# Optimization experiments

Hardware: AMD Instinct MI355X
Metric: run time of the kernel (lower is better)

## Reference

```python
import jax, jax.numpy as jnp
import numpy as np
from jax import lax

OUT_SCALE = 0.001


def setup_inputs() -> dict:
    key = jax.random.key(0)
    kz, kx = jax.random.split(key)
    z = jax.random.normal(kz, (64, 256, 7, 7), dtype=jnp.float32)
    x = jax.random.normal(kx, (64, 256, 31, 31), dtype=jnp.float32)
    return {"z": z, "x": x}


def reference(z, x):
    # depthwise cross-correlation: each (batch, channel) slice of z is slid
    # over the matching slice of x. Implemented as a grouped conv with
    # feature_group_count = B*C, exactly mirroring torch F.conv2d(groups=B*C).
    B, C, kh, kw = z.shape
    H, W = x.shape[2], x.shape[3]
    x_r = x.reshape(1, B * C, H, W)           # [1, B*C, H, W]
    k_r = z.reshape(B * C, 1, kh, kw)          # [B*C, 1, kh, kw] (OIHW)
    out = lax.conv_general_dilated(
        x_r, k_r,
        window_strides=(1, 1),
        padding="VALID",
        feature_group_count=B * C,
        dimension_numbers=("NCHW", "OIHW", "NCHW"),
    )  # [1, B*C, H-kh+1, W-kw+1]
    out = out.reshape(B, C, out.shape[2], out.shape[3])
    return out * OUT_SCALE
```

## Files before the change

### kernel.cpp

```cpp
#include <hip/hip_runtime.h>


#define KH 7
#define KW 7
#define XH 31
#define XW 31
#define OH 25
#define OW 25
#define NSLICE (64 * 256)
#define THREADS 128
#define NPAIR (NSLICE / 2)
#define NBLK 1280
#define NWAVE (NBLK * 2)
#define BUF_DW 2048
#define SLICE_X (XH * XW)
#define SLICE_O (OH * OW)
#define X_TOTAL_DW (NSLICE * SLICE_X)

__device__ __forceinline__ void gl_lds16(const float* g, float* l) {
    __builtin_amdgcn_global_load_lds(
        (const __attribute__((address_space(1))) void*)g,
        (__attribute__((address_space(3))) void*)l, 16, 0, 0);
}

__device__ __forceinline__ void stage_pair(const float* __restrict__ x,
                                           float* __restrict__ buf,
                                           int pair, int lane) {
    const int g0r = pair * (2 * SLICE_X);
    const int g0  = g0r - (g0r & 3);
    #pragma unroll
    for (int k = 0; k < 8; ++k) {
        const int dw  = k * 256 + lane * 4;
        const int gdw = min(g0 + dw, X_TOTAL_DW - 4);
        gl_lds16(x + gdw, buf + dw);
    }
}

__device__ __forceinline__ void compute_slice(float* __restrict__ buf,
                                              const float* __restrict__ zsl,
                                              int pre, int s,
                                              int oy, int c0, bool act) {
    float wz[KH * KW];
    #pragma unroll
    for (int t = 0; t < KH * KW; ++t) wz[t] = zsl[t];
    if (act) {
        float acc[13] = {};
        const float* __restrict__ xrow = buf + pre + s * SLICE_X;
        #pragma unroll
        for (int i = 0; i < KH; ++i) {
            const float* __restrict__ p = xrow + (oy + i) * XW + c0;
            float f[19];
            #pragma unroll
            for (int c = 0; c < 19; ++c) f[c] = p[c];
            #pragma unroll
            for (int j = 0; j < KW; ++j) {
                const float w = wz[i * KW + j];
                #pragma unroll
                for (int c = 0; c < 13; ++c)
                    acc[c] = fmaf(f[c + j], w, acc[c]);
            }
        }
        const int fb = s * SLICE_O + oy * OW + c0;
        #pragma unroll
        for (int c = 0; c < 12; ++c) buf[fb + c] = acc[c] * 0.001f;
        if (c0 == 0) buf[fb + 12] = acc[12] * 0.001f;
    }
}

__global__ __launch_bounds__(THREADS, 4)
void xcorr_dw_kernel(const float* __restrict__ z,
                     const float* __restrict__ x,
                     float* __restrict__ out) {
    __shared__ float xs[2][2][BUF_DW];
    const int tid  = threadIdx.x;
    const int lane = tid & 63;
    const int wv   = __builtin_amdgcn_readfirstlane(tid >> 6);
    const int wid  = blockIdx.x * 2 + wv;

    const int h   = (lane >= OH) ? 1 : 0;
    const int oy  = h ? (lane - OH) : lane;
    const int c0  = h ? 13 : 0;
    const bool act = (lane < 2 * OH);

    float* b0 = xs[wv][0];
    float* b1 = xs[wv][1];

    stage_pair(x, b0, wid, lane);
    if (wid + NWAVE < NPAIR) stage_pair(x, b1, wid + NWAVE, lane);

    #pragma unroll 1
    for (int p = wid; p < NPAIR; p += NWAVE) {
        asm volatile("s_waitcnt vmcnt(8)" ::: "memory");
        __builtin_amdgcn_sched_barrier(0);

        const int wslice = 2 * p;
        const int pre    = (2 * p) & 3;
        const float* __restrict__ zp = z + (size_t)wslice * (KH * KW);

        compute_slice(b0, zp,           pre, 0, oy, c0, act);
        compute_slice(b0, zp + KH * KW, pre, 1, oy, c0, act);

        float* __restrict__ og = out + (size_t)wslice * SLICE_O;
        #pragma unroll
        for (int k = 0; k < 19; ++k) og[k * 64 + lane] = b0[k * 64 + lane];
        if (lane < 2 * SLICE_O - 19 * 64) og[19 * 64 + lane] = b0[19 * 64 + lane];

        asm volatile("s_waitcnt lgkmcnt(0)" ::: "memory");
        __builtin_amdgcn_sched_barrier(0);
        if (p + 2 * NWAVE < NPAIR) stage_pair(x, b0, p + 2 * NWAVE, lane);

        float* t = b0; b0 = b1; b1 = t;
    }
}

extern "C" void kernel_launch(void* const* d_in, const int* in_sizes, int n_in,
                              void* d_out, int out_size, void* d_ws, size_t ws_size,
                              hipStream_t stream) {
    const float* z = (const float*)d_in[0];
    const float* x = (const float*)d_in[1];
    float* out = (float*)d_out;
    xcorr_dw_kernel<<<dim3(NBLK), dim3(THREADS), 0, stream>>>(z, x, out);
}
```

Before: 125.2 us.

## Stage one slice per wave instead of pairs, doubling blocks and occupancy

Each wave now handles one 31x31 slice per iteration instead of a pair, so the LDS buffer is halved and the grid is doubled to 2560 blocks with launch bounds raised to 5 blocks per CU. Filter weights are read straight from global memory inside the FMA loop instead of being preloaded into 49 registers, which lowers register pressure. The first iteration is peeled and out-of-range prefetches are clamped to slice 0 rather than skipped. The vmcnt waits are retuned to account for the output stores now issued inside the loop. The goal is more concurrent waves to hide memory latency, at the cost of extra always-issued dummy loads and weight loads that may not be hoisted out of the unrolled loop.

After: 116.2 us. 1.08x faster.

```diff
diff --git a/kernel.cpp b/kernel.cpp
--- a/kernel.cpp
+++ b/kernel.cpp
@@ -3,17 +3,15 @@
 
 #define KH 7
 #define KW 7
-#define XH 31
 #define XW 31
 #define OH 25
 #define OW 25
 #define NSLICE (64 * 256)
 #define THREADS 128
-#define NPAIR (NSLICE / 2)
-#define NBLK 1280
-#define NWAVE (NBLK * 2)
-#define BUF_DW 2048
-#define SLICE_X (XH * XW)
+#define NBLK 2560
+#define NWAVES (NBLK * 2)
+#define BUF_DW 1024
+#define SLICE_X (XW * XW)
 #define SLICE_O (OH * OW)
 #define X_TOTAL_DW (NSLICE * SLICE_X)
 
@@ -23,29 +21,27 @@
         (__attribute__((address_space(3))) void*)l, 16, 0, 0);
 }
 
-__device__ __forceinline__ void stage_pair(const float* __restrict__ x,
-                                           float* __restrict__ buf,
-                                           int pair, int lane) {
-    const int g0r = pair * (2 * SLICE_X);
-    const int g0  = g0r - (g0r & 3);
+__device__ __forceinline__ void stage_slice(const float* __restrict__ x,
+                                            float* __restrict__ buf,
+                                            int slice, int lane) {
+    const int g0 = (slice * SLICE_X) & ~3;
     #pragma unroll
-    for (int k = 0; k < 8; ++k) {
-        const int dw  = k * 256 + lane * 4;
-        const int gdw = min(g0 + dw, X_TOTAL_DW - 4);
-        gl_lds16(x + gdw, buf + dw);
+    for (int k = 0; k < 4; ++k) {
+        const int dw = k * 256 + lane * 4;
+        gl_lds16(x + min(g0 + dw, X_TOTAL_DW - 4), buf + dw);
     }
 }
 
-__device__ __forceinline__ void compute_slice(float* __restrict__ buf,
-                                              const float* __restrict__ zsl,
-                                              int pre, int s,
+__device__ __forceinline__ void process_slice(float* __restrict__ buf,
+                                              const float* __restrict__ z,
+                                              float* __restrict__ out,
+                                              int slice, int lane,
                                               int oy, int c0, bool act) {
-    float wz[KH * KW];
-    #pragma unroll
-    for (int t = 0; t < KH * KW; ++t) wz[t] = zsl[t];
+    const int pre = (slice * SLICE_X) & 3;
+    const float* __restrict__ zw = z + (size_t)slice * (KH * KW);
     if (act) {
         float acc[13] = {};
-        const float* __restrict__ xrow = buf + pre + s * SLICE_X;
+        const float* __restrict__ xrow = buf + pre;
         #pragma unroll
         for (int i = 0; i < KH; ++i) {
             const float* __restrict__ p = xrow + (oy + i) * XW + c0;
@@ -54,63 +50,67 @@
             for (int c = 0; c < 19; ++c) f[c] = p[c];
             #pragma unroll
             for (int j = 0; j < KW; ++j) {
-                const float w = wz[i * KW + j];
+                const float w = zw[i * KW + j];
                 #pragma unroll
                 for (int c = 0; c < 13; ++c)
                     acc[c] = fmaf(f[c + j], w, acc[c]);
             }
         }
-        const int fb = s * SLICE_O + oy * OW + c0;
+        const int fb = oy * OW + c0;
         #pragma unroll
         for (int c = 0; c < 12; ++c) buf[fb + c] = acc[c] * 0.001f;
         if (c0 == 0) buf[fb + 12] = acc[12] * 0.001f;
     }
+    float* __restrict__ og = out + (size_t)slice * SLICE_O;
+    #pragma unroll
+    for (int k = 0; k < 9; ++k) og[k * 64 + lane] = buf[k * 64 + lane];
+    if (lane < SLICE_O - 576) og[576 + lane] = buf[576 + lane];
 }
 
-__global__ __launch_bounds__(THREADS, 4)
+__global__ __launch_bounds__(THREADS, 5)
 void xcorr_dw_kernel(const float* __restrict__ z,
                      const float* __restrict__ x,
                      float* __restrict__ out) {
     __shared__ float xs[2][2][BUF_DW];
-    const int tid  = threadIdx.x;
-    const int lane = tid & 63;
-    const int wv   = __builtin_amdgcn_readfirstlane(tid >> 6);
+    const int lane = threadIdx.x & 63;
+    const int wv   = __builtin_amdgcn_readfirstlane(threadIdx.x >> 6);
     const int wid  = blockIdx.x * 2 + wv;
 
     const int h   = (lane >= OH) ? 1 : 0;
-    const int oy  = h ? (lane - OH) : lane;
+    const int oy  = h ? lane - OH : lane;
     const int c0  = h ? 13 : 0;
     const bool act = (lane < 2 * OH);
 
-    float* b0 = xs[wv][0];
-    float* b1 = xs[wv][1];
+    float* bcur = xs[wv][0];
+    float* bnxt = xs[wv][1];
 
-    stage_pair(x, b0, wid, lane);
-    if (wid + NWAVE < NPAIR) stage_pair(x, b1, wid + NWAVE, lane);
+    stage_slice(x, bcur, wid, lane);
+    stage_slice(x, bnxt, wid + NWAVES, lane);
+
+    asm volatile("s_waitcnt vmcnt(4)" ::: "memory");
+    __builtin_amdgcn_sched_barrier(0);
+    process_slice(bcur, z, out, wid, lane, oy, c0, act);
+    asm volatile("s_waitcnt lgkmcnt(0)" ::: "memory");
+    __builtin_amdgcn_sched_barrier(0);
+    {
+        const int s2 = wid + 2 * NWAVES;
+        stage_slice(x, bcur, s2 < NSLICE ? s2 : 0, lane);
+    }
+    { float* t = bcur; bcur = bnxt; bnxt = t; }
 
     #pragma unroll 1
-    for (int p = wid; p < NPAIR; p += NWAVE) {
-        asm volatile("s_waitcnt vmcnt(8)" ::: "memory");
+    for (int p = wid + NWAVES; p < NSLICE; p += NWAVES) {
+        asm volatile("s_waitcnt vmcnt(14)" ::: "memory");
         __builtin_amdgcn_sched_barrier(0);
-
-        const int wslice = 2 * p;
-        const int pre    = (2 * p) & 3;
-        const float* __restrict__ zp = z + (size_t)wslice * (KH * KW);
-
-        compute_slice(b0, zp,           pre, 0, oy, c0, act);
-        compute_slice(b0, zp + KH * KW, pre, 1, oy, c0, act);
-
-        float* __restrict__ og = out + (size_t)wslice * SLICE_O;
-        #pragma unroll
-        for (int k = 0; k < 19; ++k) og[k * 64 + lane] = b0[k * 64 + lane];
-        if (lane < 2 * SLICE_O - 19 * 64) og[19 * 64 + lane] = b0[19 * 64 + lane];
-
+        process_slice(bcur, z, out, p, lane, oy, c0, act);
         asm volatile("s_waitcnt lgkmcnt(0)" ::: "memory");
         __builtin_amdgcn_sched_barrier(0);
-        if (p + 2 * NWAVE < NPAIR) stage_pair(x, b0, p + 2 * NWAVE, lane);
+        const int s2 = p + 2 * NWAVES;
+        stage_slice(x, bcur, s2 < NSLICE ? s2 : 0, lane);
+        float* t = bcur; bcur = bnxt; bnxt = t;
+    }
 
-        float* t = b0; b0 = b1; b1 = t;
-    }
+    asm volatile("s_waitcnt vmcnt(0)" ::: "memory");
 }
 
 extern "C" void kernel_launch(void* const* d_in, const int* in_sizes, int n_in,
```
